# Kernel tuning notes

Hardware: AMD Instinct MI355X
Metric: run time of the kernel (lower is better)

Reference implementation:

```python
import jax, jax.numpy as jnp
import numpy as np

B_SZ, SEQ_LEN, STATE_DIM, D_IN, D_OUT, KX = 8, 2048, 1024, 512, 512, 10


def setup_inputs() -> dict:
    key = jax.random.key(0)
    ks = jax.random.split(key, 7)
    inputs = jax.random.normal(ks[0], (B_SZ, SEQ_LEN, D_IN), dtype=jnp.float32)
    h0 = jax.random.normal(ks[1], (STATE_DIM,), dtype=jnp.float32)
    # exponential_decay_init(lam=15): x = clamp(-1/lam * log(1-u), max=1); A = (1-x)*sign
    u = jax.random.uniform(ks[2], (STATE_DIM,), dtype=jnp.float32)
    x = jnp.minimum(-(1.0 / 15.0) * jnp.log1p(-u), 1.0)
    sign = jnp.sign(jax.random.normal(ks[3], (STATE_DIM,), dtype=jnp.float32))
    A = (1.0 - x) * sign
    Bm = jax.random.normal(ks[4], (D_IN, STATE_DIM), dtype=jnp.float32) / D_IN
    C = jax.random.normal(ks[5], (STATE_DIM, D_OUT), dtype=jnp.float32) / STATE_DIM
    M = jax.random.normal(ks[6], (D_OUT, D_IN, KX), dtype=jnp.float32) / D_OUT
    return {"inputs": inputs, "h0": h0, "A": A, "B": Bm, "C": C, "M": M}


def _ar_preds(M, x):
    # Equivalent to einsum('oik,bli->bklo') + per-k roll + triu mask + sum over k:
    # ar[b,l,:] = sum_{i=0}^{k-1, i<=l} M[:,:,i] @ x[b, l-i, :]
    b, l, d_in = x.shape
    kx = M.shape[2]
    ar = jnp.einsum('oi,bli->blo', M[:, :, 0], x)
    for i in range(1, kx):
        x_shift = jnp.pad(x, ((0, 0), (i, 0), (0, 0)))[:, :l]  # shift right, zero-fill
        ar = ar + jnp.einsum('oi,bli->blo', M[:, :, i], x_shift)
    return ar


def reference(inputs, h0, A, B, C, M):
    b, l, d_in = inputs.shape
    state_dim = A.shape[0]
    # Project inputs once: u_t @ B for all t -> [b, l, s]
    uB = jnp.einsum('bli,is->bls', inputs, B)

    def step(h, u_t):
        h = A * h + u_t  # diagonal recurrence
        return h, h

    h_init = jnp.broadcast_to(h0, (b, state_dim))
    _, hs = jax.lax.scan(step, h_init, jnp.swapaxes(uB, 0, 1))  # [l, b, s]
    hs = jnp.swapaxes(hs, 0, 1)  # [b, l, s]
    lds_out = hs @ C  # [b, l, d_out]
    return lds_out + _ar_preds(M, inputs)
```

## Files before the change

kernel.cpp:

```cpp
#include <hip/hip_runtime.h>

#define B_SZ   8
#define SEQ    2048
#define PSEQ   (SEQ+16)
#define SDIM   1024
#define DIN    512
#define DOUT   512
#define KX     10
#define RTOT   (B_SZ*SEQ)
#define LC     64
#define NC     (SEQ/LC)

typedef __attribute__((ext_vector_type(8))) short short8;
typedef __attribute__((ext_vector_type(4))) float f32x4;
typedef __attribute__((ext_vector_type(4))) unsigned short bfx4;

#define OFF_XP   0UL
#define OFF_UB   16908288UL
#define OFF_HS   50462720UL
#define OFF_BT   84017152UL
#define OFF_CT   85065728UL
#define OFF_MT   86114304UL

__device__ __forceinline__ short f2bf(float f) {
  unsigned u = __builtin_bit_cast(unsigned, f);
  u += 0x7fffu + ((u >> 16) & 1u);
  return (short)(u >> 16);
}
__device__ __forceinline__ float bf2f(unsigned short b) {
  return __builtin_bit_cast(float, (unsigned)b << 16);
}

#define GLOAD16(gp, lp) __builtin_amdgcn_global_load_lds( \
    (const __attribute__((address_space(1))) void*)(gp), \
    (__attribute__((address_space(3))) void*)(lp), 16, 0, 0)
#define WAITVM(n) asm volatile("s_waitcnt vmcnt(" #n ")" ::: "memory")
#define SBAR() __builtin_amdgcn_s_barrier()

__global__ void k_conv_x(const float* __restrict__ in, short* __restrict__ out) {
  const int NG = RTOT * (DIN / 8);
  for (int g = blockIdx.x * 256 + threadIdx.x; g < NG; g += 2048 * 256) {
    int r = g >> 6, c8 = g & 63;
    int b = r >> 11, t = r & 2047;
    const float4* p = reinterpret_cast<const float4*>(in) + (size_t)g * 2;
    float4 f0 = p[0], f1 = p[1];
    short8 o;
    o[0]=f2bf(f0.x); o[1]=f2bf(f0.y); o[2]=f2bf(f0.z); o[3]=f2bf(f0.w);
    o[4]=f2bf(f1.x); o[5]=f2bf(f1.y); o[6]=f2bf(f1.z); o[7]=f2bf(f1.w);
    *reinterpret_cast<short8*>(out + ((size_t)(b * PSEQ + 16 + t) * DIN + c8 * 8)) = o;
  }
}

__global__ void k_zero_pad(short* __restrict__ Xp) {
  int idx = blockIdx.x * 256 + threadIdx.x;
  if (idx >= B_SZ * 16 * (DIN / 8)) return;
  int b = idx >> 10, rem = idx & 1023;
  int row16 = rem >> 6, c8 = rem & 63;
  const short8 z = {0,0,0,0,0,0,0,0};
  *reinterpret_cast<short8*>(Xp + ((size_t)(b * PSEQ + row16) * DIN + c8 * 8)) = z;
}

__global__ void k_transpose_bf16(const float* __restrict__ in, short* __restrict__ out,
                                 int rows, int cols) {
  __shared__ float t[32][33];
  int bx = blockIdx.x * 32, by = blockIdx.y * 32;
  int tx = threadIdx.x & 31, ty = threadIdx.x >> 5;
  #pragma unroll
  for (int j = 0; j < 32; j += 8)
    t[ty + j][tx] = in[(size_t)(by + ty + j) * cols + (bx + tx)];
  __syncthreads();
  #pragma unroll
  for (int j = 0; j < 32; j += 8)
    out[(size_t)(bx + ty + j) * rows + (by + tx)] = f2bf(t[tx][ty + j]);
}

__global__ void k_prep_M(const float* __restrict__ M, short* __restrict__ Mt) {
  int idx = blockIdx.x * 256 + threadIdx.x;
  if (idx >= DOUT * DIN) return;
  int o = idx / DIN, i = idx - o * DIN;
  const float* src = M + ((size_t)o * DIN + i) * KX;
  #pragma unroll
  for (int t = 0; t < KX; ++t)
    Mt[((size_t)t * DOUT + o) * DIN + i] = f2bf(src[t]);
}

__global__ void k_scan_E(const short* __restrict__ uB, const float* __restrict__ A,
                         float* __restrict__ E) {
  int blk = blockIdx.x, tid = threadIdx.x;
  int b = blk >> 5, c = blk & 31;
  int s0 = tid * 4;
  const short* base = uB + ((size_t)b * SEQ + (size_t)c * LC) * SDIM + s0;
  float a[4], h[4];
  #pragma unroll
  for (int j = 0; j < 4; ++j) { a[j] = A[s0 + j]; h[j] = 0.f; }
  for (int t = 0; t < LC; ++t) {
    bfx4 v = *reinterpret_cast<const bfx4*>(base + (size_t)t * SDIM);
    #pragma unroll
    for (int j = 0; j < 4; ++j) h[j] = fmaf(a[j], h[j], bf2f(v[j]));
  }
  float* ep = E + (size_t)blk * SDIM + s0;
  #pragma unroll
  for (int j = 0; j < 4; ++j) ep[j] = h[j];
}

__global__ void k_scan_S(const float* __restrict__ E, const float* __restrict__ A,
                         const float* __restrict__ h0, float* __restrict__ Sb) {
  int blk = blockIdx.x, tid = threadIdx.x;
  int b = blk >> 2;
  int s = ((blk & 3) << 8) + tid;
  float a = A[s], ap = a;
  #pragma unroll
  for (int q = 0; q < 6; ++q) ap *= ap;
  float S = h0[s];
  for (int c = 0; c < NC; ++c) {
    size_t idx = ((size_t)b * NC + c) * SDIM + s;
    Sb[idx] = S;
    S = fmaf(ap, S, E[idx]);
  }
}

__global__ void k_scan_h(const short* __restrict__ uB, const float* __restrict__ A,
                         const float* __restrict__ Sb, short* __restrict__ hs) {
  int blk = blockIdx.x, tid = threadIdx.x;
  int b = blk >> 5, c = blk & 31;
  int s0 = tid * 4;
  const short* base = uB + ((size_t)b * SEQ + (size_t)c * LC) * SDIM + s0;
  short* hbase = hs + ((size_t)b * SEQ + (size_t)c * LC) * SDIM + s0;
  float a[4], h[4];
  #pragma unroll
  for (int j = 0; j < 4; ++j) {
    a[j] = A[s0 + j];
    h[j] = Sb[(size_t)blk * SDIM + s0 + j];
  }
  for (int t = 0; t < LC; ++t) {
    bfx4 v = *reinterpret_cast<const bfx4*>(base + (size_t)t * SDIM);
    bfx4 o;
    #pragma unroll
    for (int j = 0; j < 4; ++j) {
      h[j] = fmaf(a[j], h[j], bf2f(v[j]));
      o[j] = (unsigned short)f2bf(h[j]);
    }
    *reinterpret_cast<bfx4*>(hbase + (size_t)t * SDIM) = o;
  }
}

__device__ __forceinline__ void stage128(const short* __restrict__ g, int ld,
                                         short* l, int tid) {
  int rsub = tid >> 3;
  int slot = (tid & 7) ^ (rsub & 7);
  #pragma unroll
  for (int i = 0; i < 4; ++i) {
    int row = i * 32 + rsub;
    GLOAD16(g + (size_t)row * ld + slot * 8, l + row * 64 + (tid & 7) * 8);
  }
}
__device__ __forceinline__ void stage144(const short* __restrict__ g, int ld,
                                         short* l, int tid) {
  stage128(g, ld, l, tid);
  if (tid < 128) {
    int rsub = tid >> 3;
    int slot = (tid & 7) ^ (rsub & 7);
    int row = 128 + rsub;
    GLOAD16(g + (size_t)row * ld + slot * 8, l + row * 64 + (tid & 7) * 8);
  }
}

__device__ __forceinline__ void mfma_tile(const short* lA, int aoff, const short* lB,
                                          int lane, int wm, int wn, f32x4 acc[4][4]) {
  int lr = lane & 15;
  int h  = lane >> 4;
  #pragma unroll
  for (int kk = 0; kk < 2; ++kk) {
    int kslot = kk * 4 + h;
    short8 af[4], bfr[4];
    #pragma unroll
    for (int mi = 0; mi < 4; ++mi) {
      int row = aoff + wm * 64 + mi * 16 + lr;
      af[mi] = *reinterpret_cast<const short8*>(lA + row * 64 + ((kslot ^ (row & 7)) << 3));
    }
    #pragma unroll
    for (int ni = 0; ni < 4; ++ni) {
      int row = wn * 64 + ni * 16 + lr;
      bfr[ni] = *reinterpret_cast<const short8*>(lB + row * 64 + ((kslot ^ (row & 7)) << 3));
    }
    __builtin_amdgcn_s_setprio(1);
    #pragma unroll
    for (int mi = 0; mi < 4; ++mi)
      #pragma unroll
      for (int ni = 0; ni < 4; ++ni)
        acc[mi][ni] = __builtin_amdgcn_mfma_f32_16x16x32_bf16(af[mi], bfr[ni], acc[mi][ni], 0, 0, 0);
    __builtin_amdgcn_s_setprio(0);
  }
}

__global__ __launch_bounds__(256) void k_gemm_uB(const short* __restrict__ Xp,
                                                 const short* __restrict__ Bt,
                                                 short* __restrict__ uB) {
  __shared__ __attribute__((aligned(16))) short lds[32768];
  short* A0 = lds;         short* B0 = lds + 8192;
  short* A1 = lds + 16384; short* B1 = lds + 24576;
  int tid = threadIdx.x, lane = tid & 63, w = tid >> 6, wm = w >> 1, wn = w & 1;
  long r0 = (long)blockIdx.x * 128;
  int  c0 = blockIdx.y * 128;
  int  b  = (int)(r0 >> 11);
  const short* Abase = Xp + (size_t)(r0 + 16 * (b + 1)) * DIN;
  const short* Bbase = Bt + (size_t)c0 * DIN;
  const f32x4 z4 = {0.f, 0.f, 0.f, 0.f};
  f32x4 acc[4][4];
  #pragma unroll
  for (int mi = 0; mi < 4; ++mi)
    #pragma unroll
    for (int ni = 0; ni < 4; ++ni) acc[mi][ni] = z4;

  stage128(Abase, DIN, A0, tid);      stage128(Bbase, DIN, B0, tid);
  stage128(Abase + 64, DIN, A1, tid); stage128(Bbase + 64, DIN, B1, tid);
  WAITVM(8);
  SBAR();
  for (int kt = 0; kt < 8; ++kt) {
    const short* a  = (kt & 1) ? A1 : A0;
    const short* bb = (kt & 1) ? B1 : B0;
    mfma_tile(a, 0, bb, lane, wm, wn, acc);
    SBAR();
    if (kt + 2 < 8) {
      short* ad = (kt & 1) ? A1 : A0;
      short* bd = (kt & 1) ? B1 : B0;
      stage128(Abase + (kt + 2) * 64, DIN, ad, tid);
      stage128(Bbase + (kt + 2) * 64, DIN, bd, tid);
      WAITVM(8);
    } else {
      WAITVM(0);
    }
    SBAR();
  }
  #pragma unroll
  for (int mi = 0; mi < 4; ++mi)
    #pragma unroll
    for (int ni = 0; ni < 4; ++ni)
      #pragma unroll
      for (int r = 0; r < 4; ++r) {
        long row = r0 + wm * 64 + mi * 16 + (lane >> 4) * 4 + r;
        int  col = c0 + wn * 64 + ni * 16 + (lane & 15);
        uB[(size_t)row * SDIM + col] = f2bf(acc[mi][ni][r]);
      }
}

__global__ __launch_bounds__(256) void k_gemm_out(const short* __restrict__ hs,
                                                  const short* __restrict__ Xp,
                                                  const short* __restrict__ Ct,
                                                  const short* __restrict__ Mt,
                                                  float* __restrict__ out) {
  __shared__ __attribute__((aligned(16))) short lds[32768];
  short* A0 = lds;         short* B0 = lds + 8192;
  short* A1 = lds + 16384; short* B1 = lds + 24576;
  short* Xs = lds;
  short* M0 = lds + 16384;
  short* M1 = lds + 24576;
  int tid = threadIdx.x, lane = tid & 63, w = tid >> 6, wm = w >> 1, wn = w & 1;
  long r0 = (long)blockIdx.x * 128;
  int  c0 = blockIdx.y * 128;
  int  b  = (int)(r0 >> 11);
  const short* hsA = hs + (size_t)r0 * SDIM;
  const short* CtB = Ct + (size_t)c0 * SDIM;
  const short* Xa  = Xp + (size_t)(r0 + 16 * (b + 1) - 16) * DIN;
  const f32x4 z4 = {0.f, 0.f, 0.f, 0.f};
  f32x4 acc[4][4];
  #pragma unroll
  for (int mi = 0; mi < 4; ++mi)
    #pragma unroll
    for (int ni = 0; ni < 4; ++ni) acc[mi][ni] = z4;

  stage128(hsA, SDIM, A0, tid);      stage128(CtB, SDIM, B0, tid);
  stage128(hsA + 64, SDIM, A1, tid); stage128(CtB + 64, SDIM, B1, tid);
  WAITVM(8);
  SBAR();
  for (int kt = 0; kt < 16; ++kt) {
    const short* a  = (kt & 1) ? A1 : A0;
    const short* bb = (kt & 1) ? B1 : B0;
    mfma_tile(a, 0, bb, lane, wm, wn, acc);
    SBAR();
    if (kt + 2 < 16) {
      short* ad = (kt & 1) ? A1 : A0;
      short* bd = (kt & 1) ? B1 : B0;
      stage128(hsA + (kt + 2) * 64, SDIM, ad, tid);
      stage128(CtB + (kt + 2) * 64, SDIM, bd, tid);
      WAITVM(8);
    } else {
      WAITVM(0);
    }
    SBAR();
  }

  for (int k0 = 0; k0 < 8; ++k0) {
    int kc = k0 * 64;
    stage144(Xa + kc, DIN, Xs, tid);
    stage128(Mt + (size_t)c0 * DIN + kc, DIN, M0, tid);
    stage128(Mt + (size_t)DOUT * DIN + (size_t)c0 * DIN + kc, DIN, M1, tid);
    WAITVM(4);
    SBAR();
    for (int tap = 0; tap < KX; ++tap) {
      const short* mb = (tap & 1) ? M1 : M0;
      mfma_tile(Xs, 16 - tap, mb, lane, wm, wn, acc);
      SBAR();
      if (tap + 2 < KX) {
        short* md = (tap & 1) ? M1 : M0;
        stage128(Mt + (size_t)(tap + 2) * DOUT * DIN + (size_t)c0 * DIN + kc, DIN, md, tid);
        WAITVM(4);
      } else {
        WAITVM(0);
      }
      SBAR();
    }
  }

  #pragma unroll
  for (int mi = 0; mi < 4; ++mi)
    #pragma unroll
    for (int ni = 0; ni < 4; ++ni)
      #pragma unroll
      for (int r = 0; r < 4; ++r) {
        long row = r0 + wm * 64 + mi * 16 + (lane >> 4) * 4 + r;
        int  col = c0 + wn * 64 + ni * 16 + (lane & 15);
        out[(size_t)row * DOUT + col] = acc[mi][ni][r];
      }
}

extern "C" void kernel_launch(void* const* d_in, const int* in_sizes, int n_in,
                              void* d_out, int out_size, void* d_ws, size_t ws_size,
                              hipStream_t stream) {
  (void)in_sizes; (void)n_in; (void)out_size; (void)ws_size;
  const float* x  = (const float*)d_in[0];
  const float* h0 = (const float*)d_in[1];
  const float* A  = (const float*)d_in[2];
  const float* B  = (const float*)d_in[3];
  const float* C  = (const float*)d_in[4];
  const float* M  = (const float*)d_in[5];
  float* out = (float*)d_out;
  char* ws = (char*)d_ws;

  short* Xp  = (short*)(ws + OFF_XP);
  short* uB  = (short*)(ws + OFF_UB);
  short* hsb = (short*)(ws + OFF_HS);
  short* Bt  = (short*)(ws + OFF_BT);
  short* Ct  = (short*)(ws + OFF_CT);
  short* Mt  = (short*)(ws + OFF_MT);
  float* E   = out;
  float* Sb  = out + B_SZ * NC * SDIM;

  k_conv_x<<<2048, 256, 0, stream>>>(x, Xp);
  k_zero_pad<<<32, 256, 0, stream>>>(Xp);
  k_transpose_bf16<<<dim3(SDIM / 32, DIN / 32), 256, 0, stream>>>(B, Bt, DIN, SDIM);
  k_transpose_bf16<<<dim3(DOUT / 32, SDIM / 32), 256, 0, stream>>>(C, Ct, SDIM, DOUT);
  k_prep_M<<<(DOUT * DIN + 255) / 256, 256, 0, stream>>>(M, Mt);

  k_gemm_uB<<<dim3(RTOT / 128, SDIM / 128), 256, 0, stream>>>(Xp, Bt, uB);

  k_scan_E<<<B_SZ * NC, 256, 0, stream>>>(uB, A, E);
  k_scan_S<<<B_SZ * 4, 256, 0, stream>>>(E, A, h0, Sb);
  k_scan_h<<<B_SZ * NC, 256, 0, stream>>>(uB, A, Sb, hsb);

  k_gemm_out<<<dim3(RTOT / 128, DOUT / 128), 256, 0, stream>>>(hsb, Xp, Ct, Mt, out);
}
```

Measured before the change: 156.0 us.

## Enlarge output GEMM tile to 256x128 with 512 threads and swizzled grid

```diff
diff --git a/kernel.cpp b/kernel.cpp
--- a/kernel.cpp
+++ b/kernel.cpp
@@ -35,6 +35,8 @@
     (const __attribute__((address_space(1))) void*)(gp), \
     (__attribute__((address_space(3))) void*)(lp), 16, 0, 0)
 #define WAITVM(n) asm volatile("s_waitcnt vmcnt(" #n ")" ::: "memory")
+#define LGKM0()   do { asm volatile("s_waitcnt lgkmcnt(0)" ::: "memory"); \
+                       __builtin_amdgcn_sched_barrier(0); } while (0)
 #define SBAR() __builtin_amdgcn_s_barrier()
 
 __global__ void k_conv_x(const float* __restrict__ in, short* __restrict__ out) {
@@ -151,16 +153,6 @@
   #pragma unroll
   for (int i = 0; i < 4; ++i) {
     int row = i * 32 + rsub;
-    GLOAD16(g + (size_t)row * ld + slot * 8, l + row * 64 + (tid & 7) * 8);
-  }
-}
-__device__ __forceinline__ void stage144(const short* __restrict__ g, int ld,
-                                         short* l, int tid) {
-  stage128(g, ld, l, tid);
-  if (tid < 128) {
-    int rsub = tid >> 3;
-    int slot = (tid & 7) ^ (rsub & 7);
-    int row = 128 + rsub;
     GLOAD16(g + (size_t)row * ld + slot * 8, l + row * 64 + (tid & 7) * 8);
   }
 }
@@ -244,24 +236,90 @@
       }
 }
 
-__global__ __launch_bounds__(256) void k_gemm_out(const short* __restrict__ hs,
+
+__device__ __forceinline__ void stageA256(const short* __restrict__ g, int ld,
+                                          short* l, int tid) {
+  int rsub = tid >> 3;
+  int slot = (tid & 7) ^ (rsub & 7);
+  #pragma unroll
+  for (int i = 0; i < 4; ++i) {
+    int row = i * 64 + rsub;
+    GLOAD16(g + (size_t)row * ld + slot * 8, l + row * 64 + (tid & 7) * 8);
+  }
+}
+__device__ __forceinline__ void stageB128(const short* __restrict__ g, int ld,
+                                          short* l, int tid) {
+  int rsub = tid >> 3;
+  int slot = (tid & 7) ^ (rsub & 7);
+  #pragma unroll
+  for (int i = 0; i < 2; ++i) {
+    int row = i * 64 + rsub;
+    GLOAD16(g + (size_t)row * ld + slot * 8, l + row * 64 + (tid & 7) * 8);
+  }
+}
+__device__ __forceinline__ void stageX272(const short* __restrict__ g, int ld,
+                                          short* l, int tid) {
+  stageA256(g, ld, l, tid);
+  if (tid < 128) {
+    int rsub = tid >> 3;
+    int row = 256 + rsub;
+    int slot = (tid & 7) ^ (row & 7);
+    GLOAD16(g + (size_t)row * ld + slot * 8, l + row * 64 + (tid & 7) * 8);
+  }
+}
+
+__device__ __forceinline__ void compute_step(const short* la, int aoff, const short* lb,
+                                             int lane, int wm, int wn, f32x4 acc[4][4]) {
+  int lr = lane & 15;
+  int h  = lane >> 4;
+  short8 af[4][2], bfr[4][2];
+  #pragma unroll
+  for (int kk = 0; kk < 2; ++kk) {
+    int kslot = kk * 4 + h;
+    #pragma unroll
+    for (int mi = 0; mi < 4; ++mi) {
+      int row = aoff + wm * 64 + mi * 16 + lr;
+      af[mi][kk] = *reinterpret_cast<const short8*>(la + row * 64 + ((kslot ^ (row & 7)) << 3));
+    }
+    #pragma unroll
+    for (int ni = 0; ni < 4; ++ni) {
+      int row = wn * 64 + ni * 16 + lr;
+      bfr[ni][kk] = *reinterpret_cast<const short8*>(lb + row * 64 + ((kslot ^ (row & 7)) << 3));
+    }
+  }
+  __builtin_amdgcn_s_setprio(1);
+  #pragma unroll
+  for (int kk = 0; kk < 2; ++kk)
+    #pragma unroll
+    for (int mi = 0; mi < 4; ++mi)
+      #pragma unroll
+      for (int ni = 0; ni < 4; ++ni)
+        acc[mi][ni] = __builtin_amdgcn_mfma_f32_16x16x32_bf16(af[mi][kk], bfr[ni][kk], acc[mi][ni], 0, 0, 0);
+  __builtin_amdgcn_s_setprio(0);
+}
+
+__global__ __launch_bounds__(512) void k_gemm_out(const short* __restrict__ hs,
                                                   const short* __restrict__ Xp,
                                                   const short* __restrict__ Ct,
                                                   const short* __restrict__ Mt,
                                                   float* __restrict__ out) {
-  __shared__ __attribute__((aligned(16))) short lds[32768];
-  short* A0 = lds;         short* B0 = lds + 8192;
-  short* A1 = lds + 16384; short* B1 = lds + 24576;
-  short* Xs = lds;
-  short* M0 = lds + 16384;
-  short* M1 = lds + 24576;
-  int tid = threadIdx.x, lane = tid & 63, w = tid >> 6, wm = w >> 1, wn = w & 1;
-  long r0 = (long)blockIdx.x * 128;
-  int  c0 = blockIdx.y * 128;
+  __shared__ __attribute__((aligned(16))) short lds[49152];
+  short* A0p = lds;          short* B0p = lds + 16384;
+  short* A1p = lds + 24576;  short* B1p = lds + 40960;
+  short* Xs  = lds;
+  short* M0p = lds + 24576;  short* M1p = lds + 40960;
+  int tid = threadIdx.x, lane = tid & 63, w = tid >> 6;
+  int wm = w >> 1, wn = w & 1;
+  int bid = blockIdx.x;
+  int sw  = (bid & 7) * 32 + (bid >> 3);
+  long r0 = (long)(sw & 63) * 256;
+  int  c0 = (sw >> 6) * 128;
   int  b  = (int)(r0 >> 11);
   const short* hsA = hs + (size_t)r0 * SDIM;
   const short* CtB = Ct + (size_t)c0 * SDIM;
   const short* Xa  = Xp + (size_t)(r0 + 16 * (b + 1) - 16) * DIN;
+  const short* MtB = Mt + (size_t)c0 * DIN;
+
   const f32x4 z4 = {0.f, 0.f, 0.f, 0.f};
   f32x4 acc[4][4];
   #pragma unroll
@@ -269,45 +327,47 @@
     #pragma unroll
     for (int ni = 0; ni < 4; ++ni) acc[mi][ni] = z4;
 
-  stage128(hsA, SDIM, A0, tid);      stage128(CtB, SDIM, B0, tid);
-  stage128(hsA + 64, SDIM, A1, tid); stage128(CtB + 64, SDIM, B1, tid);
-  WAITVM(8);
+  stageA256(hsA, SDIM, A0p, tid);
+  stageB128(CtB, SDIM, B0p, tid);
+  WAITVM(0);
   SBAR();
-  for (int kt = 0; kt < 16; ++kt) {
-    const short* a  = (kt & 1) ? A1 : A0;
-    const short* bb = (kt & 1) ? B1 : B0;
-    mfma_tile(a, 0, bb, lane, wm, wn, acc);
+  for (int s = 0; s < 16; ++s) {
+    const short* la = (s & 1) ? A1p : A0p;
+    const short* lb = (s & 1) ? B1p : B0p;
+    short* na = (s & 1) ? A0p : A1p;
+    short* nb = (s & 1) ? B0p : B1p;
+    if (s + 1 < 16) {
+      stageA256(hsA + (s + 1) * 64, SDIM, na, tid);
+      stageB128(CtB + (s + 1) * 64, SDIM, nb, tid);
+    } else {
+      stageX272(Xa, DIN, Xs, tid);
+    }
+    compute_step(la, 0, lb, lane, wm, wn, acc);
+    LGKM0();
+    WAITVM(0);
     SBAR();
-    if (kt + 2 < 16) {
-      short* ad = (kt & 1) ? A1 : A0;
-      short* bd = (kt & 1) ? B1 : B0;
-      stage128(hsA + (kt + 2) * 64, SDIM, ad, tid);
-      stage128(CtB + (kt + 2) * 64, SDIM, bd, tid);
-      WAITVM(8);
-    } else {
-      WAITVM(0);
-    }
-    SBAR();
-  }
-
+  }
+
+  stageB128(MtB, DIN, M0p, tid);
+  WAITVM(0);
+  SBAR();
   for (int k0 = 0; k0 < 8; ++k0) {
     int kc = k0 * 64;
-    stage144(Xa + kc, DIN, Xs, tid);
-    stage128(Mt + (size_t)c0 * DIN + kc, DIN, M0, tid);
-    stage128(Mt + (size_t)DOUT * DIN + (size_t)c0 * DIN + kc, DIN, M1, tid);
-    WAITVM(4);
-    SBAR();
     for (int tap = 0; tap < KX; ++tap) {
-      const short* mb = (tap & 1) ? M1 : M0;
-      mfma_tile(Xs, 16 - tap, mb, lane, wm, wn, acc);
+      const short* lm = (tap & 1) ? M1p : M0p;
+      short* nm = (tap & 1) ? M0p : M1p;
+      if (tap + 1 < KX)
+        stageB128(MtB + (size_t)(tap + 1) * DOUT * DIN + kc, DIN, nm, tid);
+      else if (k0 + 1 < 8)
+        stageB128(MtB + kc + 64, DIN, M0p, tid);
+      compute_step(Xs, 16 - tap, lm, lane, wm, wn, acc);
+      LGKM0();
+      WAITVM(0);
       SBAR();
-      if (tap + 2 < KX) {
-        short* md = (tap & 1) ? M1 : M0;
-        stage128(Mt + (size_t)(tap + 2) * DOUT * DIN + (size_t)c0 * DIN + kc, DIN, md, tid);
-        WAITVM(4);
-      } else {
-        WAITVM(0);
-      }
+    }
+    if (k0 + 1 < 8) {
+      stageX272(Xa + kc + 64, DIN, Xs, tid);
+      WAITVM(0);
       SBAR();
     }
   }
@@ -358,5 +418,5 @@
   k_scan_S<<<B_SZ * 4, 256, 0, stream>>>(E, A, h0, Sb);
   k_scan_h<<<B_SZ * NC, 256, 0, stream>>>(uB, A, Sb, hsb);
 
-  k_gemm_out<<<dim3(RTOT / 128, DOUT / 128), 256, 0, stream>>>(hsb, Xp, Ct, Mt, out);
-}
+  k_gemm_out<<<256, 512, 0, stream>>>(hsb, Xp, Ct, Mt, out);
+}
```

Result: no change. 156.4 us (+0.2%).
